# Kernel tuning notes

Hardware: AMD Instinct MI355X
Metric: run time of the kernel (lower is better)

## Reference

```python
import jax, jax.numpy as jnp
import numpy as np
from functools import partial

ALPHA = 2.0  # surrogate sharpness

@partial(jax.custom_vjp, nondiff_argnums=(1,))
def spike(x, alpha):
    # Heaviside forward, atan surrogate backward
    return (x >= 0.0).astype(x.dtype)

def _spike_fwd(x, alpha):
    return spike(x, alpha), x

def _spike_bwd(alpha, x, g):
    grad = (alpha / 2.0) / (1.0 + (jnp.pi / 2.0 * alpha * x) ** 2)
    return (g * grad,)

spike.defvjp(_spike_fwd, _spike_bwd)


def setup_inputs() -> dict:
    key = jax.random.key(0)
    k1, k2, k3 = jax.random.split(key, 3)
    B, T, H = 128, 2048, 512
    TAU_INIT, TH_INIT = 8.0, 0.5
    x_seq = jax.random.normal(k1, (B, T, 2), dtype=jnp.float32)
    W_in = jax.random.normal(k2, (2, H), dtype=jnp.float32) * (1.0 / np.sqrt(2.0))
    b_in = jnp.zeros((H,), dtype=jnp.float32)
    # PLIF: sigmoid(w_tau) = 1/tau  =>  w_tau = -log(tau - 1)
    w_tau = jnp.full((H,), -np.log(TAU_INIT - 1.0), dtype=jnp.float32)
    threshold = jnp.full((H,), TH_INIT, dtype=jnp.float32)
    W_out = jax.random.normal(k3, (H, 2), dtype=jnp.float32) * (1.0 / np.sqrt(H))
    b_out = jnp.zeros((2,), dtype=jnp.float32)
    return {"x_seq": x_seq, "W_in": W_in, "b_in": b_in,
            "w_tau": w_tau, "threshold": threshold,
            "W_out": W_out, "b_out": b_out}


def reference(x_seq, W_in, b_in, w_tau, threshold, W_out, b_out):
    B, T, _ = x_seq.shape
    H = W_in.shape[1]
    cur = x_seq @ W_in + b_in                      # [B, T, H]
    decay = jax.nn.sigmoid(w_tau)                  # [H], = 1/tau

    def step(v, c):
        v = v + (c - v) * decay                    # leaky integration
        s = spike(v - threshold, ALPHA)            # threshold + surrogate
        v = v * (1.0 - s)                          # hard reset
        return v, s

    v0 = jnp.zeros((B, H), dtype=x_seq.dtype)
    _, s_seq = jax.lax.scan(step, v0, jnp.transpose(cur, (1, 0, 2)))  # s_seq: [T, B, H]
    rate = s_seq.mean(axis=0)                      # [B, H]
    return rate @ W_out + b_out                    # [B, 2]
```

## Files before the change

kernel.cpp:

```cpp
#include <hip/hip_runtime.h>
#include <math.h>

#define NB 128
#define NT 2048
#define NH 512
#define HBLK 64
#define HCHUNKS (NH / HBLK)

__global__ void init_out_kernel(const float* __restrict__ b_out,
                                float* __restrict__ out) {
    int i = blockIdx.x * blockDim.x + threadIdx.x;
    if (i < NB * 2) out[i] = b_out[i & 1];
}

__global__ __launch_bounds__(HBLK, 1)
void snn_scan_kernel(const float* __restrict__ x,
                     const float* __restrict__ W_in,
                     const float* __restrict__ b_in,
                     const float* __restrict__ w_tau,
                     const float* __restrict__ thr_p,
                     const float* __restrict__ W_out,
                     float* __restrict__ out) {
    __shared__ float4 xs[NT / 2];

    const int blk = blockIdx.x;
    const int b   = blk >> 3;
    const int hc  = blk & 7;
    const int h   = hc * HBLK + threadIdx.x;

    const float4* __restrict__ xb =
        (const float4*)(x + (size_t)b * (NT * 2));
    #pragma unroll
    for (int i = 0; i < 16; ++i)
        xs[i * HBLK + threadIdx.x] = xb[i * HBLK + threadIdx.x];

    const float w0 = W_in[h];
    const float w1 = W_in[NH + h];
    const float bi = b_in[h];
    const float wt = w_tau[h];
    const float decay = (wt >= 0.0f)
        ? (1.0f / (1.0f + expf(-wt)))
        : ({ float e = expf(wt); e / (1.0f + e); });
    const float th = thr_p[h];

    const float A0 = w0 * decay;
    const float A1 = w1 * decay;
    const float Bd = bi * decay;
    const float K  = 1.0f - decay;

    __syncthreads();

    float vp = 0.0f;
    bool  sp = false;
    int   cnt = 0;

    float4 c0 = xs[0], c1 = xs[1], c2 = xs[2], c3 = xs[3];

    for (int it = 0; it < NT / 8; ++it) {
        const int nx = ((it + 1) & (NT / 8 - 1)) * 4;
        float4 n0 = xs[nx + 0];
        float4 n1 = xs[nx + 1];
        float4 n2 = xs[nx + 2];
        float4 n3 = xs[nx + 3];

        float xv[16] = { c0.x, c0.y, c0.z, c0.w,
                         c1.x, c1.y, c1.z, c1.w,
                         c2.x, c2.y, c2.z, c2.w,
                         c3.x, c3.y, c3.z, c3.w };
        #pragma unroll
        for (int k = 0; k < 8; ++k) {
            float cd = fmaf(xv[2 * k], A0, fmaf(xv[2 * k + 1], A1, Bd));
            float vn = fmaf(vp, K, cd);
            vp = sp ? cd : vn;
            sp = (vp >= th);
            cnt += sp ? 1 : 0;
        }

        c0 = n0; c1 = n1; c2 = n2; c3 = n3;
    }

    float rate = (float)cnt * (1.0f / (float)NT);
    float o0 = rate * W_out[2 * h];
    float o1 = rate * W_out[2 * h + 1];

    #pragma unroll
    for (int off = 32; off > 0; off >>= 1) {
        o0 += __shfl_down(o0, off, 64);
        o1 += __shfl_down(o1, off, 64);
    }
    if (threadIdx.x == 0) {
        atomicAdd(&out[b * 2 + 0], o0);
        atomicAdd(&out[b * 2 + 1], o1);
    }
}

extern "C" void kernel_launch(void* const* d_in, const int* in_sizes, int n_in,
                              void* d_out, int out_size, void* d_ws, size_t ws_size,
                              hipStream_t stream) {
    const float* x     = (const float*)d_in[0];
    const float* W_in  = (const float*)d_in[1];
    const float* b_in  = (const float*)d_in[2];
    const float* w_tau = (const float*)d_in[3];
    const float* thr   = (const float*)d_in[4];
    const float* W_out = (const float*)d_in[5];
    const float* b_out = (const float*)d_in[6];
    float* out = (float*)d_out;

    hipLaunchKernelGGL(init_out_kernel, dim3(1), dim3(256), 0, stream,
                       b_out, out);
    hipLaunchKernelGGL(snn_scan_kernel, dim3(NB * HCHUNKS), dim3(HBLK), 0, stream,
                       x, W_in, b_in, w_tau, thr, W_out, out);
}
```

Baseline: 102.5 us.

## Deepen LDS prefetch, unroll scan loop, add sched barriers, fold bias into atomics

The scan loop now processes 16 timesteps per iteration with 8 float4 prefetches of the next chunk from LDS, plus unroll 2 and sched_group_barrier hints that interleave the LDS reads with the VALU chain. The init kernel that wrote b_out into the output is replaced by a memset, and the hc==0 block adds the bias before its atomic add. The aim is to hide LDS latency behind the serial recurrence and cut a small kernel launch, at the cost of more registers and a scheduling hint that may not fit the real instruction counts.

Result: no change. 101.7 us (-0.8%).

```diff
diff --git a/kernel.cpp b/kernel.cpp
--- a/kernel.cpp
+++ b/kernel.cpp
@@ -7,11 +7,19 @@
 #define HBLK 64
 #define HCHUNKS (NH / HBLK)
 
-__global__ void init_out_kernel(const float* __restrict__ b_out,
-                                float* __restrict__ out) {
-    int i = blockIdx.x * blockDim.x + threadIdx.x;
-    if (i < NB * 2) out[i] = b_out[i & 1];
-}
+#define STEP2(q)                                                  \
+    do {                                                          \
+        float cdA = fmaf((q).x, A0, fmaf((q).y, A1, Bd));         \
+        float vnA = fmaf(vp, K, cdA);                             \
+        vp = sp ? cdA : vnA;                                      \
+        sp = (vp >= th);                                          \
+        cnt += sp ? 1 : 0;                                        \
+        float cdB = fmaf((q).z, A0, fmaf((q).w, A1, Bd));         \
+        float vnB = fmaf(vp, K, cdB);                             \
+        vp = sp ? cdB : vnB;                                      \
+        sp = (vp >= th);                                          \
+        cnt += sp ? 1 : 0;                                        \
+    } while (0)
 
 __global__ __launch_bounds__(HBLK, 1)
 void snn_scan_kernel(const float* __restrict__ x,
@@ -20,6 +28,7 @@
                      const float* __restrict__ w_tau,
                      const float* __restrict__ thr_p,
                      const float* __restrict__ W_out,
+                     const float* __restrict__ b_out,
                      float* __restrict__ out) {
     __shared__ float4 xs[NT / 2];
 
@@ -55,28 +64,28 @@
     int   cnt = 0;
 
     float4 c0 = xs[0], c1 = xs[1], c2 = xs[2], c3 = xs[3];
+    float4 c4 = xs[4], c5 = xs[5], c6 = xs[6], c7 = xs[7];
 
-    for (int it = 0; it < NT / 8; ++it) {
-        const int nx = ((it + 1) & (NT / 8 - 1)) * 4;
+    #pragma unroll 2
+    for (int it = 0; it < NT / 16; ++it) {
+        const int nx = ((it + 1) & (NT / 16 - 1)) * 8;
         float4 n0 = xs[nx + 0];
         float4 n1 = xs[nx + 1];
         float4 n2 = xs[nx + 2];
         float4 n3 = xs[nx + 3];
+        float4 n4 = xs[nx + 4];
+        float4 n5 = xs[nx + 5];
+        float4 n6 = xs[nx + 6];
+        float4 n7 = xs[nx + 7];
 
-        float xv[16] = { c0.x, c0.y, c0.z, c0.w,
-                         c1.x, c1.y, c1.z, c1.w,
-                         c2.x, c2.y, c2.z, c2.w,
-                         c3.x, c3.y, c3.z, c3.w };
-        #pragma unroll
-        for (int k = 0; k < 8; ++k) {
-            float cd = fmaf(xv[2 * k], A0, fmaf(xv[2 * k + 1], A1, Bd));
-            float vn = fmaf(vp, K, cd);
-            vp = sp ? cd : vn;
-            sp = (vp >= th);
-            cnt += sp ? 1 : 0;
-        }
+        STEP2(c0); STEP2(c1); STEP2(c2); STEP2(c3);
+        STEP2(c4); STEP2(c5); STEP2(c6); STEP2(c7);
+
+        __builtin_amdgcn_sched_group_barrier(0x100, 8, 0);
+        __builtin_amdgcn_sched_group_barrier(0x002, 112, 0);
 
         c0 = n0; c1 = n1; c2 = n2; c3 = n3;
+        c4 = n4; c5 = n5; c6 = n6; c7 = n7;
     }
 
     float rate = (float)cnt * (1.0f / (float)NT);
@@ -89,6 +98,10 @@
         o1 += __shfl_down(o1, off, 64);
     }
     if (threadIdx.x == 0) {
+        if (hc == 0) {
+            o0 += b_out[0];
+            o1 += b_out[1];
+        }
         atomicAdd(&out[b * 2 + 0], o0);
         atomicAdd(&out[b * 2 + 1], o1);
     }
@@ -106,8 +119,7 @@
     const float* b_out = (const float*)d_in[6];
     float* out = (float*)d_out;
 
-    hipLaunchKernelGGL(init_out_kernel, dim3(1), dim3(256), 0, stream,
-                       b_out, out);
+    hipMemsetAsync(out, 0, (size_t)out_size * sizeof(float), stream);
     hipLaunchKernelGGL(snn_scan_kernel, dim3(NB * HCHUNKS), dim3(HBLK), 0, stream,
-                       x, W_in, b_in, w_tau, thr, W_out, out);
+                       x, W_in, b_in, w_tau, thr, W_out, b_out, out);
 }
```
